# Performance work log

Measured on AMD Instinct MI355X. Metric: run time of the kernel, lower is better.

## Reference

```python
import jax, jax.numpy as jnp
import numpy as np

BETA = 0.25  # commitment weight from __init__ default
K, D = 512, 64


def setup_inputs() -> dict:
    key = jax.random.key(0)
    k1, k2 = jax.random.split(key)
    latents = jax.random.normal(k1, (32, 64, 64, 64), dtype=jnp.float32)  # [B, D, H, W]
    # nn.Embedding weight initialized uniform(-1/K, 1/K)
    emb_weight = jax.random.uniform(k2, (K, D), dtype=jnp.float32, minval=-1.0 / K, maxval=1.0 / K)
    return {"latents": latents, "emb_weight": emb_weight, "validation": 1}


def reference(latents, emb_weight, validation):
    B, Dc, H, W = latents.shape
    lat = jnp.transpose(latents, (0, 2, 3, 1))          # [B, H, W, D]
    flat = lat.reshape(-1, Dc)                           # [N, D]
    # pairwise squared distances via sum-of-squares + matmul (as in source)
    dist = (jnp.sum(flat * flat, axis=1, keepdims=True)
            + jnp.sum(emb_weight * emb_weight, axis=1)
            - 2.0 * flat @ emb_weight.T)                 # [N, K]
    inds = jnp.argmin(dist, axis=1)                      # [N]
    # one_hot @ emb_weight == gather
    q = emb_weight[inds].reshape(B, H, W, Dc)            # [B, H, W, D]
    commitment_loss = jnp.mean((jax.lax.stop_gradient(q) - lat) ** 2)
    embedding_loss = jnp.mean((q - jax.lax.stop_gradient(lat)) ** 2)
    # eloss starts at 0.0 (and stays 0 in validation), so topology terms vanish
    vq_loss = commitment_loss * BETA + embedding_loss
    # straight-through estimator
    q_st = lat + jax.lax.stop_gradient(q - lat)
    return jnp.transpose(q_st, (0, 3, 1, 2)), vq_loss
```

## Files before the change

### kernel.cpp

```cpp
#include <hip/hip_runtime.h>


typedef __bf16 bf16_t;
typedef __attribute__((ext_vector_type(8))) __bf16 bf16x8;
typedef __attribute__((ext_vector_type(16))) float floatx16;

namespace {
constexpr int K    = 512;
constexpr int D    = 64;
constexpr int HW   = 4096;
constexpr int NPIX = 32 * HW;
constexpr int QOUT = NPIX * D;
constexpr int DEXT = 80;
}

__global__ __launch_bounds__(64) void vq_prep(const float* __restrict__ emb,
                                              bf16_t* __restrict__ ext,
                                              float* __restrict__ loss) {
    int k = blockIdx.x * 64 + threadIdx.x;
    if (k == 0) *loss = 0.0f;
    if (k >= K) return;
    const float4* row = (const float4*)(emb + k * D);
    float4 v[16];
#pragma unroll
    for (int i = 0; i < 16; ++i) v[i] = row[i];
    float s = 0.0f;
#pragma unroll
    for (int i = 0; i < 16; ++i)
        s += v[i].x * v[i].x + v[i].y * v[i].y + v[i].z * v[i].z + v[i].w * v[i].w;
    bf16_t r[DEXT];
#pragma unroll
    for (int i = 0; i < 16; ++i) {
        r[4 * i + 0] = (bf16_t)v[i].x;
        r[4 * i + 1] = (bf16_t)v[i].y;
        r[4 * i + 2] = (bf16_t)v[i].z;
        r[4 * i + 3] = (bf16_t)v[i].w;
    }
    r[64] = (bf16_t)(-0.5f * s);
#pragma unroll
    for (int i = 65; i < DEXT; ++i) r[i] = (bf16_t)0.0f;
#pragma unroll
    for (int i = 0; i < DEXT / 8; ++i)
        ((bf16x8*)(ext + k * DEXT))[i] = *(const bf16x8*)(r + 8 * i);
}

__global__ __launch_bounds__(256) void vq_mfma(
    const float* __restrict__ lat,
    const float* __restrict__ emb,
    const bf16_t* __restrict__ ext,
    float* __restrict__ out,
    float* __restrict__ loss) {
    const int lane = threadIdx.x & 63;
    const int wave = threadIdx.x >> 6;
    const int col  = lane & 31;
    const int half = lane >> 5;
    const unsigned h4 = (unsigned)(half << 2);
    const int nb   = blockIdx.x * 256 + wave * 64;

    const int n0 = nb + 2 * col;
    const int b  = n0 >> 12;
    const int hw = n0 & (HW - 1);
    const float* latp = lat + (size_t)b * D * HW + hw;

    bf16x8 bfrag[2][5];
#pragma unroll
    for (int s = 0; s < 4; ++s) {
#pragma unroll
        for (int j = 0; j < 8; ++j) {
            int d = s * 16 + half * 8 + j;
            float2 v = *(const float2*)(latp + (size_t)d * HW);
            bfrag[0][s][j] = (bf16_t)v.x;
            bfrag[1][s][j] = (bf16_t)v.y;
        }
    }
#pragma unroll
    for (int j = 0; j < 8; ++j) {
        bfrag[0][4][j] = (bf16_t)0.0f;
        bfrag[1][4][j] = (bf16_t)0.0f;
    }
    if (half == 0) {
        bfrag[0][4][0] = (bf16_t)1.0f;
        bfrag[1][4][0] = (bf16_t)1.0f;
    }

    unsigned best0 = 0u, best1 = 0u;

#pragma unroll 4
    for (int t = 0; t < 16; ++t) {
        const bf16_t* arow = ext + ((size_t)(t * 32 + col)) * DEXT + half * 8;
        bf16x8 af[5];
#pragma unroll
        for (int s = 0; s < 5; ++s) af[s] = *(const bf16x8*)(arow + s * 16);

        floatx16 acc0, acc1;
#pragma unroll
        for (int r = 0; r < 16; ++r) { acc0[r] = 1.0f; acc1[r] = 1.0f; }
#pragma unroll
        for (int s = 0; s < 5; ++s)
            acc0 = __builtin_amdgcn_mfma_f32_32x32x16_bf16(af[s], bfrag[0][s], acc0, 0, 0, 0);
#pragma unroll
        for (int s = 0; s < 5; ++s)
            acc1 = __builtin_amdgcn_mfma_f32_32x32x16_bf16(af[s], bfrag[1][s], acc1, 0, 0, 0);

#pragma unroll
        for (int r = 0; r < 16; ++r) {
            unsigned codebase = (unsigned)(t * 32 + ((r & 3) + 8 * (r >> 2)));
            unsigned c0 = (__float_as_uint(acc0[r]) & 0xFFFFFE00u) | codebase | h4;
            unsigned c1 = (__float_as_uint(acc1[r]) & 0xFFFFFE00u) | codebase | h4;
            best0 = best0 > c0 ? best0 : c0;
            best1 = best1 > c1 ? best1 : c1;
        }
    }

    {
        unsigned o0 = (unsigned)__shfl_xor((int)best0, 32, 64);
        unsigned o1 = (unsigned)__shfl_xor((int)best1, 32, 64);
        best0 = best0 > o0 ? best0 : o0;
        best1 = best1 > o1 ? best1 : o1;
    }
    const int k0 = (int)(best0 & 511u);
    const int k1 = (int)(best1 & 511u);

    const float* e0 = emb + k0 * D + half * 8;
    const float* e1 = emb + k1 * D + half * 8;
    float* outp = out + (size_t)b * D * HW + hw;
    float sqtot = 0.0f;
#pragma unroll
    for (int s = 0; s < 4; ++s) {
        float4 a0 = *(const float4*)(e0 + s * 16);
        float4 a1 = *(const float4*)(e0 + s * 16 + 4);
        float4 c0 = *(const float4*)(e1 + s * 16);
        float4 c1 = *(const float4*)(e1 + s * 16 + 4);
        float q0[8] = {a0.x, a0.y, a0.z, a0.w, a1.x, a1.y, a1.z, a1.w};
        float q1[8] = {c0.x, c0.y, c0.z, c0.w, c1.x, c1.y, c1.z, c1.w};
#pragma unroll
        for (int j = 0; j < 8; ++j) {
            float x0 = (float)bfrag[0][s][j];
            float x1 = (float)bfrag[1][s][j];
            float d0 = q0[j] - x0;
            float d1 = q1[j] - x1;
            sqtot += d0 * d0 + d1 * d1;
            int d = s * 16 + half * 8 + j;
            *(float2*)(outp + (size_t)d * HW) = make_float2(q0[j], q1[j]);
        }
    }

#pragma unroll
    for (int off = 32; off > 0; off >>= 1) sqtot += __shfl_down(sqtot, off, 64);
    __shared__ float part[4];
    if (lane == 0) part[wave] = sqtot;
    __syncthreads();
    if (threadIdx.x == 0) {
        float t = part[0] + part[1] + part[2] + part[3];
        atomicAdd(loss, t * (1.25f / (float)QOUT));
    }
}

extern "C" void kernel_launch(void* const* d_in, const int* in_sizes, int n_in,
                              void* d_out, int out_size, void* d_ws, size_t ws_size,
                              hipStream_t stream) {
    const float* lat = (const float*)d_in[0];
    const float* emb = (const float*)d_in[1];
    float* out       = (float*)d_out;
    float* loss      = out + QOUT;
    bf16_t* ext      = (bf16_t*)d_ws;

    vq_prep<<<K / 64, 64, 0, stream>>>(emb, ext, loss);
    vq_mfma<<<NPIX / 256, 256, 0, stream>>>(lat, emb, ext, out, loss);
}
```

Before: 106.6 us.

## Stage codebook in LDS, process two pixel tiles per wave, derive loss from scores

```diff
diff --git a/kernel.cpp b/kernel.cpp
--- a/kernel.cpp
+++ b/kernel.cpp
@@ -4,6 +4,7 @@
 typedef __bf16 bf16_t;
 typedef __attribute__((ext_vector_type(8))) __bf16 bf16x8;
 typedef __attribute__((ext_vector_type(16))) float floatx16;
+typedef __attribute__((ext_vector_type(4))) float floatx4;
 
 namespace {
 constexpr int K    = 512;
@@ -11,11 +12,15 @@
 constexpr int HW   = 4096;
 constexpr int NPIX = 32 * HW;
 constexpr int QOUT = NPIX * D;
-constexpr int DEXT = 80;
+constexpr int ROWB = 144;
+constexpr int EXT_BYTES  = K * ROWB;
+constexpr int BIAS_OFF   = EXT_BYTES;
+constexpr int SMEM_BYTES = EXT_BYTES + K * 4;
+constexpr int SMEM_CHUNKS = SMEM_BYTES / 1024;
 }
 
 __global__ __launch_bounds__(64) void vq_prep(const float* __restrict__ emb,
-                                              bf16_t* __restrict__ ext,
+                                              char* __restrict__ ws,
                                               float* __restrict__ loss) {
     int k = blockIdx.x * 64 + threadIdx.x;
     if (k == 0) *loss = 0.0f;
@@ -28,7 +33,7 @@
 #pragma unroll
     for (int i = 0; i < 16; ++i)
         s += v[i].x * v[i].x + v[i].y * v[i].y + v[i].z * v[i].z + v[i].w * v[i].w;
-    bf16_t r[DEXT];
+    bf16_t r[72];
 #pragma unroll
     for (int i = 0; i < 16; ++i) {
         r[4 * i + 0] = (bf16_t)v[i].x;
@@ -36,114 +41,186 @@
         r[4 * i + 2] = (bf16_t)v[i].z;
         r[4 * i + 3] = (bf16_t)v[i].w;
     }
-    r[64] = (bf16_t)(-0.5f * s);
-#pragma unroll
-    for (int i = 65; i < DEXT; ++i) r[i] = (bf16_t)0.0f;
-#pragma unroll
-    for (int i = 0; i < DEXT / 8; ++i)
-        ((bf16x8*)(ext + k * DEXT))[i] = *(const bf16x8*)(r + 8 * i);
+#pragma unroll
+    for (int i = 64; i < 72; ++i) r[i] = (bf16_t)0.0f;
+    bf16_t* dst = (bf16_t*)(ws + (size_t)k * ROWB);
+#pragma unroll
+    for (int i = 0; i < 9; ++i)
+        ((bf16x8*)dst)[i] = *(const bf16x8*)(r + 8 * i);
+    ((float*)(ws + BIAS_OFF))[k] = 1.0f - 0.5f * s;
 }
 
 __global__ __launch_bounds__(256) void vq_mfma(
     const float* __restrict__ lat,
     const float* __restrict__ emb,
-    const bf16_t* __restrict__ ext,
+    const char* __restrict__ wsrc,
     float* __restrict__ out,
     float* __restrict__ loss) {
+    __shared__ char smem[SMEM_BYTES];
+
     const int lane = threadIdx.x & 63;
     const int wave = threadIdx.x >> 6;
     const int col  = lane & 31;
     const int half = lane >> 5;
     const unsigned h4 = (unsigned)(half << 2);
-    const int nb   = blockIdx.x * 256 + wave * 64;
-
-    const int n0 = nb + 2 * col;
+
+    for (int c = wave; c < SMEM_CHUNKS; c += 4) {
+        __builtin_amdgcn_global_load_lds(
+            (const __attribute__((address_space(1))) unsigned int*)(wsrc + c * 1024 + lane * 16),
+            (__attribute__((address_space(3))) unsigned int*)(smem + c * 1024),
+            16, 0, 0);
+    }
+    __syncthreads();
+
+    const int w  = blockIdx.x * 4 + wave;
+    const int n0 = w * 128 + 2 * col;
     const int b  = n0 >> 12;
     const int hw = n0 & (HW - 1);
     const float* latp = lat + (size_t)b * D * HW + hw;
 
-    bf16x8 bfrag[2][5];
-#pragma unroll
-    for (int s = 0; s < 4; ++s) {
-#pragma unroll
-        for (int j = 0; j < 8; ++j) {
-            int d = s * 16 + half * 8 + j;
-            float2 v = *(const float2*)(latp + (size_t)d * HW);
-            bfrag[0][s][j] = (bf16_t)v.x;
-            bfrag[1][s][j] = (bf16_t)v.y;
-        }
-    }
-#pragma unroll
-    for (int j = 0; j < 8; ++j) {
-        bfrag[0][4][j] = (bf16_t)0.0f;
-        bfrag[1][4][j] = (bf16_t)0.0f;
-    }
-    if (half == 0) {
-        bfrag[0][4][0] = (bf16_t)1.0f;
-        bfrag[1][4][0] = (bf16_t)1.0f;
-    }
-
-    unsigned best0 = 0u, best1 = 0u;
-
-#pragma unroll 4
-    for (int t = 0; t < 16; ++t) {
-        const bf16_t* arow = ext + ((size_t)(t * 32 + col)) * DEXT + half * 8;
-        bf16x8 af[5];
-#pragma unroll
-        for (int s = 0; s < 5; ++s) af[s] = *(const bf16x8*)(arow + s * 16);
-
-        floatx16 acc0, acc1;
-#pragma unroll
-        for (int r = 0; r < 16; ++r) { acc0[r] = 1.0f; acc1[r] = 1.0f; }
-#pragma unroll
-        for (int s = 0; s < 5; ++s)
-            acc0 = __builtin_amdgcn_mfma_f32_32x32x16_bf16(af[s], bfrag[0][s], acc0, 0, 0, 0);
-#pragma unroll
-        for (int s = 0; s < 5; ++s)
-            acc1 = __builtin_amdgcn_mfma_f32_32x32x16_bf16(af[s], bfrag[1][s], acc1, 0, 0, 0);
-
-#pragma unroll
-        for (int r = 0; r < 16; ++r) {
-            unsigned codebase = (unsigned)(t * 32 + ((r & 3) + 8 * (r >> 2)));
-            unsigned c0 = (__float_as_uint(acc0[r]) & 0xFFFFFE00u) | codebase | h4;
-            unsigned c1 = (__float_as_uint(acc1[r]) & 0xFFFFFE00u) | codebase | h4;
-            best0 = best0 > c0 ? best0 : c0;
-            best1 = best1 > c1 ? best1 : c1;
-        }
-    }
-
-    {
+    float2 rawA[32], rawB[32];
+#pragma unroll
+    for (int s = 0; s < 4; ++s)
+#pragma unroll
+        for (int j = 0; j < 8; ++j) {
+            int d = s * 16 + half * 8 + j;
+            rawA[s * 8 + j] = *(const float2*)(latp + (size_t)d * HW);
+        }
+#pragma unroll
+    for (int s = 0; s < 4; ++s)
+#pragma unroll
+        for (int j = 0; j < 8; ++j) {
+            int d = s * 16 + half * 8 + j;
+            rawB[s * 8 + j] = *(const float2*)(latp + (size_t)d * HW + 64);
+        }
+
+    bf16x8 bfA[2][4];
+    float xsqA0 = 0.0f, xsqA1 = 0.0f;
+#pragma unroll
+    for (int s = 0; s < 4; ++s)
+#pragma unroll
+        for (int j = 0; j < 8; ++j) {
+            float2 v = rawA[s * 8 + j];
+            bfA[0][s][j] = (bf16_t)v.x;
+            bfA[1][s][j] = (bf16_t)v.y;
+            xsqA0 += v.x * v.x;
+            xsqA1 += v.y * v.y;
+        }
+
+    auto tloop = [&](const bf16x8 (&bf)[2][4], unsigned& best0, unsigned& best1) {
+        best0 = 0u; best1 = 0u;
+#pragma unroll 2
+        for (int t = 0; t < 16; ++t) {
+            floatx4 bi[4];
+#pragma unroll
+            for (int c4 = 0; c4 < 4; ++c4)
+                bi[c4] = *(const floatx4*)(smem + BIAS_OFF + t * 128 + half * 16 + c4 * 32);
+            floatx16 acc0, acc1;
+#pragma unroll
+            for (int r = 0; r < 16; ++r) {
+                float bv = bi[r >> 2][r & 3];
+                acc0[r] = bv;
+                acc1[r] = bv;
+            }
+            const char* arow = smem + (size_t)(t * 32 + col) * ROWB + half * 16;
+            bf16x8 af[4];
+#pragma unroll
+            for (int s = 0; s < 4; ++s) af[s] = *(const bf16x8*)(arow + s * 32);
+#pragma unroll
+            for (int s = 0; s < 4; ++s) {
+                acc0 = __builtin_amdgcn_mfma_f32_32x32x16_bf16(af[s], bf[0][s], acc0, 0, 0, 0);
+                acc1 = __builtin_amdgcn_mfma_f32_32x32x16_bf16(af[s], bf[1][s], acc1, 0, 0, 0);
+            }
+#pragma unroll
+            for (int r = 0; r < 16; ++r) {
+                unsigned cb = (unsigned)(t * 32 + ((r & 3) + 8 * (r >> 2))) | h4;
+                unsigned c0 = (__float_as_uint(acc0[r]) & 0xFFFFFE00u) | cb;
+                unsigned c1 = (__float_as_uint(acc1[r]) & 0xFFFFFE00u) | cb;
+                best0 = best0 > c0 ? best0 : c0;
+                best1 = best1 > c1 ? best1 : c1;
+            }
+        }
         unsigned o0 = (unsigned)__shfl_xor((int)best0, 32, 64);
         unsigned o1 = (unsigned)__shfl_xor((int)best1, 32, 64);
         best0 = best0 > o0 ? best0 : o0;
         best1 = best1 > o1 ? best1 : o1;
-    }
-    const int k0 = (int)(best0 & 511u);
-    const int k1 = (int)(best1 & 511u);
-
-    const float* e0 = emb + k0 * D + half * 8;
-    const float* e1 = emb + k1 * D + half * 8;
-    float* outp = out + (size_t)b * D * HW + hw;
-    float sqtot = 0.0f;
+    };
+
+    unsigned bestA0, bestA1;
+    tloop(bfA, bestA0, bestA1);
+    const int kA0 = (int)(bestA0 & 511u), kA1 = (int)(bestA1 & 511u);
+    const float scA0 = __uint_as_float(bestA0 & 0xFFFFFE00u);
+    const float scA1 = __uint_as_float(bestA1 & 0xFFFFFE00u);
+
+    const float* eA0 = emb + kA0 * D + half * 8;
+    const float* eA1 = emb + kA1 * D + half * 8;
+    float4 qA0[8], qA1[8];
 #pragma unroll
     for (int s = 0; s < 4; ++s) {
-        float4 a0 = *(const float4*)(e0 + s * 16);
-        float4 a1 = *(const float4*)(e0 + s * 16 + 4);
-        float4 c0 = *(const float4*)(e1 + s * 16);
-        float4 c1 = *(const float4*)(e1 + s * 16 + 4);
-        float q0[8] = {a0.x, a0.y, a0.z, a0.w, a1.x, a1.y, a1.z, a1.w};
-        float q1[8] = {c0.x, c0.y, c0.z, c0.w, c1.x, c1.y, c1.z, c1.w};
-#pragma unroll
-        for (int j = 0; j < 8; ++j) {
-            float x0 = (float)bfrag[0][s][j];
-            float x1 = (float)bfrag[1][s][j];
-            float d0 = q0[j] - x0;
-            float d1 = q1[j] - x1;
-            sqtot += d0 * d0 + d1 * d1;
-            int d = s * 16 + half * 8 + j;
-            *(float2*)(outp + (size_t)d * HW) = make_float2(q0[j], q1[j]);
-        }
-    }
+        qA0[2 * s]     = *(const float4*)(eA0 + s * 16);
+        qA0[2 * s + 1] = *(const float4*)(eA0 + s * 16 + 4);
+        qA1[2 * s]     = *(const float4*)(eA1 + s * 16);
+        qA1[2 * s + 1] = *(const float4*)(eA1 + s * 16 + 4);
+    }
+
+    bf16x8 bfB[2][4];
+    float xsqB0 = 0.0f, xsqB1 = 0.0f;
+#pragma unroll
+    for (int s = 0; s < 4; ++s)
+#pragma unroll
+        for (int j = 0; j < 8; ++j) {
+            float2 v = rawB[s * 8 + j];
+            bfB[0][s][j] = (bf16_t)v.x;
+            bfB[1][s][j] = (bf16_t)v.y;
+            xsqB0 += v.x * v.x;
+            xsqB1 += v.y * v.y;
+        }
+
+    unsigned bestB0, bestB1;
+    tloop(bfB, bestB0, bestB1);
+    const int kB0 = (int)(bestB0 & 511u), kB1 = (int)(bestB1 & 511u);
+    const float scB0 = __uint_as_float(bestB0 & 0xFFFFFE00u);
+    const float scB1 = __uint_as_float(bestB1 & 0xFFFFFE00u);
+
+    float* outpA = out + (size_t)b * D * HW + hw;
+#pragma unroll
+    for (int s = 0; s < 4; ++s)
+#pragma unroll
+        for (int j = 0; j < 8; ++j) {
+            int d = s * 16 + half * 8 + j;
+            float a = (j < 4) ? qA0[2 * s][j] : qA0[2 * s + 1][j - 4];
+            float c = (j < 4) ? qA1[2 * s][j] : qA1[2 * s + 1][j - 4];
+            *(float2*)(outpA + (size_t)d * HW) = make_float2(a, c);
+        }
+
+    const float* eB0 = emb + kB0 * D + half * 8;
+    const float* eB1 = emb + kB1 * D + half * 8;
+    float4 qB0[8], qB1[8];
+#pragma unroll
+    for (int s = 0; s < 4; ++s) {
+        qB0[2 * s]     = *(const float4*)(eB0 + s * 16);
+        qB0[2 * s + 1] = *(const float4*)(eB0 + s * 16 + 4);
+        qB1[2 * s]     = *(const float4*)(eB1 + s * 16);
+        qB1[2 * s + 1] = *(const float4*)(eB1 + s * 16 + 4);
+    }
+    float* outpB = outpA + 64;
+#pragma unroll
+    for (int s = 0; s < 4; ++s)
+#pragma unroll
+        for (int j = 0; j < 8; ++j) {
+            int d = s * 16 + half * 8 + j;
+            float a = (j < 4) ? qB0[2 * s][j] : qB0[2 * s + 1][j - 4];
+            float c = (j < 4) ? qB1[2 * s][j] : qB1[2 * s + 1][j - 4];
+            *(float2*)(outpB + (size_t)d * HW) = make_float2(a, c);
+        }
+
+    float xsqA0f = xsqA0 + __shfl_xor(xsqA0, 32, 64);
+    float xsqA1f = xsqA1 + __shfl_xor(xsqA1, 32, 64);
+    float xsqB0f = xsqB0 + __shfl_xor(xsqB0, 32, 64);
+    float xsqB1f = xsqB1 + __shfl_xor(xsqB1, 32, 64);
+    float sqtot = (xsqA0f - 2.0f * (scA0 - 1.0f)) + (xsqA1f - 2.0f * (scA1 - 1.0f))
+                + (xsqB0f - 2.0f * (scB0 - 1.0f)) + (xsqB1f - 2.0f * (scB1 - 1.0f));
+    sqtot *= 0.5f;
 
 #pragma unroll
     for (int off = 32; off > 0; off >>= 1) sqtot += __shfl_down(sqtot, off, 64);
@@ -163,8 +240,8 @@
     const float* emb = (const float*)d_in[1];
     float* out       = (float*)d_out;
     float* loss      = out + QOUT;
-    bf16_t* ext      = (bf16_t*)d_ws;
-
-    vq_prep<<<K / 64, 64, 0, stream>>>(emb, ext, loss);
-    vq_mfma<<<NPIX / 256, 256, 0, stream>>>(lat, emb, ext, out, loss);
-}
+    char* ws         = (char*)d_ws;
+
+    vq_prep<<<K / 64, 64, 0, stream>>>(emb, ws, loss);
+    vq_mfma<<<256, 256, 0, stream>>>(lat, emb, ws, out, loss);
+}
```

After: 102.5 us. 1.04x faster.
